# Optimization experiments

Hardware: AMD Instinct MI355X
Metric: run time of the kernel (lower is better)

Reference implementation:

```python
import jax, jax.numpy as jnp
import numpy as np

# static config (Phi-3-like with GQA)
B, S, H, HKV, D, BS = 2, 2048, 32, 8, 128, 64
HID = H * D
NB = B * (S // BS)  # total cache blocks
THETA = 10000.0


def rotate_half(x):
    x1, x2 = jnp.split(x, 2, axis=-1)
    return jnp.concatenate([-x2, x1], axis=-1)


def rope_cos_sin(positions):
    # positions: [T] int -> cos/sin [T, D]
    inv_freq = 1.0 / (THETA ** (jnp.arange(0, D, 2, dtype=jnp.float32) / D))
    freqs = positions.astype(jnp.float32)[:, None] * inv_freq[None, :]
    emb = jnp.concatenate([freqs, freqs], axis=-1)
    return jnp.cos(emb), jnp.sin(emb)


def setup_inputs() -> dict:
    key = jax.random.key(0)
    k1, k2, k3 = jax.random.split(key, 3)
    T = B * S
    hidden_states = jax.random.normal(k1, (T, HID), dtype=jnp.float32)
    w_qkv = jax.random.normal(k2, ((H + 2 * HKV) * D, HID), dtype=jnp.float32) * 0.02
    w_o = jax.random.normal(k3, (HID, H * D), dtype=jnp.float32) * 0.02
    k_cache = jnp.zeros((NB, BS, HKV, D), dtype=jnp.float32)
    v_cache = jnp.zeros((NB, BS, HKV, D), dtype=jnp.float32)
    position_ids = jnp.tile(jnp.arange(S, dtype=jnp.int32), B)  # per-token positions (prefill)
    block_offsets = jnp.arange(NB, dtype=jnp.int32).reshape(B, S // BS)
    return dict(hidden_states=hidden_states, w_qkv=w_qkv, w_o=w_o,
                k_cache=k_cache, v_cache=v_cache, position_ids=position_ids,
                block_offsets=block_offsets, window_size=1024)


def reference(hidden_states, w_qkv, w_o, k_cache, v_cache, position_ids, block_offsets, window_size):
    # fused qkv projection + split
    qkv = hidden_states @ w_qkv.T  # [T, (H+2*HKV)*D]
    q, k, v = jnp.split(qkv, [H * D, H * D + HKV * D], axis=-1)
    q = q.reshape(-1, H, D)
    k = k.reshape(-1, HKV, D)
    v = v.reshape(-1, HKV, D)

    # rotary embedding on flattened tokens
    cos, sin = rope_cos_sin(position_ids)  # [T, D]
    cos, sin = cos[:, None, :], sin[:, None, :]
    q = q * cos + rotate_half(q) * sin
    k = k * cos + rotate_half(k) * sin

    # fill paged KV cache: token t of seq b -> block block_offsets[b, t//BS], slot t%BS
    flat_blocks = block_offsets.reshape(-1)  # [NB]
    k_blk = k.reshape(NB, BS, HKV, D)
    v_blk = v.reshape(NB, BS, HKV, D)
    k_cache = k_cache.at[flat_blocks].set(k_blk)
    v_cache = v_cache.at[flat_blocks].set(v_blk)

    # paged attention: gather per-sequence K/V through the block table
    k_seq = k_cache[block_offsets].reshape(B, S, HKV, D)
    v_seq = v_cache[block_offsets].reshape(B, S, HKV, D)

    G = H // HKV  # query heads per kv head (GQA)
    qh = q.reshape(B, S, HKV, G, D)
    scale = 1.0 / jnp.sqrt(jnp.float32(D))
    scores = jnp.einsum('bshgd,bthd->bhgst', qh, k_seq) * scale  # [B,HKV,G,S,S]

    # causal + sliding-window mask: j <= i and i - j < window_size
    i = jnp.arange(S)[:, None]
    j = jnp.arange(S)[None, :]
    mask = (j <= i) & ((i - j) < window_size)  # [S,S]
    scores = jnp.where(mask[None, None, None], scores, jnp.finfo(scores.dtype).min)
    probs = jax.nn.softmax(scores, axis=-1)

    out = jnp.einsum('bhgst,bthd->bshgd', probs, v_seq)  # [B,S,HKV,G,D]
    out = out.reshape(B * S, H * D)
    return out @ w_o.T  # [T, HID]
```

## Files before the change

### kernel.cpp

```cpp
#include <hip/hip_runtime.h>
#include <hip/hip_bf16.h>
#include <stdint.h>

typedef unsigned short u16;
typedef __attribute__((ext_vector_type(8))) short short8;
typedef __attribute__((ext_vector_type(8))) unsigned short u16x8;
typedef __attribute__((ext_vector_type(4))) float f32x4;

#define B_    2
#define S_    2048
#define H_    32
#define HKV_  8
#define D_    128
#define HID_  4096
#define QKVW_ 6144

__device__ __forceinline__ u16 f2bf(float f){
  uint32_t b = __builtin_bit_cast(uint32_t, f);
  b += 0x7FFFu + ((b >> 16) & 1u);
  return (u16)(b >> 16);
}
__device__ __forceinline__ float bf2f(u16 h){
  uint32_t b = ((uint32_t)h) << 16;
  return __builtin_bit_cast(float, b);
}
__device__ __forceinline__ u16 bfc(float f){
  __hip_bfloat16 h = __float2bfloat16(f);
  return __builtin_bit_cast(u16, h);
}

__device__ __forceinline__ void gload16(const u16* g, u16* l){
  __builtin_amdgcn_global_load_lds((const __attribute__((address_space(1))) void*)g,
                                   (__attribute__((address_space(3))) void*)l, 16, 0, 0);
}

__global__ void cvt_kernel(const float* __restrict__ src, u16* __restrict__ dst, int n4){
  int i = blockIdx.x * blockDim.x + threadIdx.x;
  int stride = gridDim.x * blockDim.x;
  for (; i < n4; i += stride){
    float4 v = reinterpret_cast<const float4*>(src)[i];
    union { u16 u[4]; unsigned long long ll; } o;
    o.u[0] = f2bf(v.x); o.u[1] = f2bf(v.y); o.u[2] = f2bf(v.z); o.u[3] = f2bf(v.w);
    reinterpret_cast<unsigned long long*>(dst)[i] = o.ll;
  }
}

__global__ void rope_table_kernel(float2* __restrict__ tab){
  int idx = blockIdx.x * blockDim.x + threadIdx.x;
  if (idx >= S_ * 64) return;
  int pos = idx >> 6, p = idx & 63;
  float inv = powf(10000.0f, -(float)p / 64.0f);
  float ang = (float)pos * inv;
  tab[idx] = make_float2(cosf(ang), sinf(ang));
}

__global__ void rope_k_kernel(u16* __restrict__ qkv, const int* __restrict__ pos_ids,
                              const float2* __restrict__ tab){
  int t = blockIdx.x;
  int pos = pos_ids[t];
  const float2* tb = tab + pos * 64;
  u16* row = qkv + (size_t)t * QKVW_ + HID_;
  for (int it = threadIdx.x; it < HKV_ * 64; it += 256){
    int hh = it >> 6, p = it & 63;
    int base = hh * D_;
    float x1 = bf2f(row[base + p]);
    float x2 = bf2f(row[base + 64 + p]);
    float2 cs = tb[p];
    row[base + p]      = f2bf(x1 * cs.x - x2 * cs.y);
    row[base + 64 + p] = f2bf(x2 * cs.x + x1 * cs.y);
  }
}

#define MFMA_(a, b, c) __builtin_amdgcn_mfma_f32_16x16x32_bf16((a), (b), (c), 0, 0, 0)

__global__ __launch_bounds__(256) void gemm128(const u16* __restrict__ A, const u16* __restrict__ B,
                                               u16* __restrict__ C, int M, int N, int K){
  __shared__ u16 As[128*64];
  __shared__ u16 Bs[128*64];
  const int tid  = threadIdx.x;
  const int wave = tid >> 6, lane = tid & 63;
  const int hi = lane >> 4, lo = lane & 15;
  const int bn = blockIdx.x, bm = blockIdx.y;
  const int wm = (wave >> 1) * 64, wn = (wave & 1) * 64;
  f32x4 acc[4][4] = {};

  const u16* ap[4]; const u16* bp[4];
  u16* lA[4]; u16* lB[4];
  #pragma unroll
  for (int p = 0; p < 4; p++){
    int e   = p*2048 + wave*512 + lane*8;
    int row = e >> 6;
    int cs  = ((e >> 3) & 7) ^ (row & 7);
    ap[p] = A + (size_t)(bm*128 + row) * K + cs*8;
    bp[p] = B + (size_t)(bn*128 + row) * K + cs*8;
    lA[p] = &As[p*2048 + wave*512];
    lB[p] = &Bs[p*2048 + wave*512];
  }
  const int sw = lo & 7;
  const int nk = K >> 6;
  for (int t = 0; t < nk; t++){
    #pragma unroll
    for (int p = 0; p < 4; p++){
      gload16(ap[p], lA[p]);
      gload16(bp[p], lB[p]);
      ap[p] += 64; bp[p] += 64;
    }
    __syncthreads();
    #pragma unroll
    for (int kk = 0; kk < 2; kk++){
      short8 af[4], bf[4];
      int sz = ((kk*4 + hi) ^ sw) * 8;
      #pragma unroll
      for (int mt = 0; mt < 4; mt++) af[mt] = *(const short8*)&As[(wm + mt*16 + lo)*64 + sz];
      #pragma unroll
      for (int nt = 0; nt < 4; nt++) bf[nt] = *(const short8*)&Bs[(wn + nt*16 + lo)*64 + sz];
      #pragma unroll
      for (int mt = 0; mt < 4; mt++)
        #pragma unroll
        for (int nt = 0; nt < 4; nt++)
          acc[mt][nt] = MFMA_(af[mt], bf[nt], acc[mt][nt]);
    }
    __syncthreads();
  }
  #pragma unroll
  for (int mt = 0; mt < 4; mt++){
    int row = bm*128 + wm + mt*16 + 4*hi;
    #pragma unroll
    for (int nt = 0; nt < 4; nt++){
      int col = bn*128 + wn + nt*16 + lo;
      #pragma unroll
      for (int r = 0; r < 4; r++)
        C[(size_t)(row + r)*N + col] = f2bf(acc[mt][nt][r]);
    }
  }
}

__global__ __launch_bounds__(512, 2) void gemm256(const u16* __restrict__ A, const u16* __restrict__ B,
                                                  float* __restrict__ C, int M, int N, int K, int nbn){
  __shared__ u16 As[2][16384];
  __shared__ u16 Bs[2][16384];
  const int tid = threadIdx.x;
  const int wave = tid >> 6, lane = tid & 63, lo = lane & 15, hi = lane >> 4;
  const int wr = wave >> 2, wc = wave & 3;
  const int sw = lo & 7;

  const int nwg = gridDim.x, bid = blockIdx.x, cpx = nwg >> 3;
  const int wg = (bid & 7) * cpx + (bid >> 3);
  const int bm = wg / nbn, bn = wg - bm * nbn;

  f32x4 acc[8][4] = {};

  const int pr0 = tid >> 3;
  const int sc0 = (tid & 7) ^ (pr0 & 7);
  const u16* aS0 = A + ((size_t)(bm*256 + pr0      ))*K + sc0*8;
  const u16* aS1 = A + ((size_t)(bm*256 + pr0 + 128))*K + sc0*8;
  const u16* aS2 = A + ((size_t)(bm*256 + pr0 + 64 ))*K + sc0*8;
  const u16* aS3 = A + ((size_t)(bm*256 + pr0 + 192))*K + sc0*8;
  const u16* bS0 = B + ((size_t)(bn*256 + pr0      ))*K + sc0*8;
  const u16* bS1 = B + ((size_t)(bn*256 + pr0 + 64 ))*K + sc0*8;
  const u16* bS2 = B + ((size_t)(bn*256 + pr0 + 128))*K + sc0*8;
  const u16* bS3 = B + ((size_t)(bn*256 + pr0 + 192))*K + sc0*8;
  const int dOfs = tid * 8;

  gload16(bS0, &Bs[0][dOfs]);        gload16(bS1, &Bs[0][4096 + dOfs]);
  gload16(bS2, &Bs[0][8192 + dOfs]); gload16(bS3, &Bs[0][12288 + dOfs]);
  gload16(aS0, &As[0][dOfs]);        gload16(aS1, &As[0][4096 + dOfs]);
  gload16(aS2, &As[0][8192 + dOfs]); gload16(aS3, &As[0][12288 + dOfs]);
  asm volatile("s_waitcnt vmcnt(0)" ::: "memory");
  __builtin_amdgcn_s_barrier();

  const int nk = K >> 6;
  for (int t = 0; t < nk; ++t){
    const int cur = t & 1, nxt = cur ^ 1;
    const u16* Ac = &As[cur][0];
    const u16* Bc = &Bs[cur][0];
    u16* An = &As[nxt][0];
    u16* Bn = &Bs[nxt][0];
    const size_t ko = (size_t)(t + 1) * 64;
    const bool more = (t + 1 < nk);
    short8 avr[4], bvr[8];

    #define RD_A(q) \
      _Pragma("unroll") for (int mt = 0; mt < 2; mt++) \
        _Pragma("unroll") for (int kk = 0; kk < 2; kk++){ \
          int ra = wr*128 + (q)*32 + mt*16 + lo; \
          int fo = ((ra & 63) << 6) + ((ra & 64) ? 8192 : 0) + ((ra & 128) ? 4096 : 0) \
                 + ((((kk << 2) + hi) ^ sw) << 3); \
          avr[mt*2 + kk] = *(const short8*)&Ac[fo]; \
        }
    #define DO_MFMA(q) \
      __builtin_amdgcn_s_setprio(1); \
      _Pragma("unroll") for (int mt = 0; mt < 2; mt++) \
        _Pragma("unroll") for (int nt = 0; nt < 4; nt++) \
          _Pragma("unroll") for (int kk = 0; kk < 2; kk++) \
            acc[(q)*2 + mt][nt] = MFMA_(avr[mt*2 + kk], bvr[nt*2 + kk], acc[(q)*2 + mt][nt]); \
      __builtin_amdgcn_s_setprio(0);

    #pragma unroll
    for (int nt = 0; nt < 4; nt++)
      #pragma unroll
      for (int kk = 0; kk < 2; kk++){
        int rb = wc*64 + nt*16 + lo;
        int fo = (rb << 6) + ((((kk << 2) + hi) ^ sw) << 3);
        bvr[nt*2 + kk] = *(const short8*)&Bc[fo];
      }
    RD_A(0)
    if (more){ gload16(bS0 + ko, Bn + dOfs); gload16(bS1 + ko, Bn + 4096 + dOfs); }
    __builtin_amdgcn_s_barrier();
    DO_MFMA(0)
    __builtin_amdgcn_s_barrier();

    RD_A(1)
    if (more){
      gload16(bS2 + ko, Bn + 8192 + dOfs); gload16(bS3 + ko, Bn + 12288 + dOfs);
      asm volatile("s_waitcnt vmcnt(4)" ::: "memory");
    } else {
      asm volatile("s_waitcnt vmcnt(0)" ::: "memory");
    }
    __builtin_amdgcn_sched_barrier(0);
    __builtin_amdgcn_s_barrier();
    DO_MFMA(1)
    __builtin_amdgcn_s_barrier();

    RD_A(2)
    if (more){ gload16(aS0 + ko, An + dOfs); gload16(aS1 + ko, An + 4096 + dOfs); }
    __builtin_amdgcn_s_barrier();
    DO_MFMA(2)
    __builtin_amdgcn_s_barrier();

    RD_A(3)
    if (more){ gload16(aS2 + ko, An + 8192 + dOfs); gload16(aS3 + ko, An + 12288 + dOfs); }
    asm volatile("s_waitcnt vmcnt(2)" ::: "memory");
    __builtin_amdgcn_sched_barrier(0);
    __builtin_amdgcn_s_barrier();
    DO_MFMA(3)
    __builtin_amdgcn_s_barrier();
    #undef RD_A
    #undef DO_MFMA
  }

  #pragma unroll
  for (int mtg = 0; mtg < 8; mtg++){
    int row = bm*256 + wr*128 + mtg*16 + 4*hi;
    #pragma unroll
    for (int nt = 0; nt < 4; nt++){
      int col = bn*256 + wc*64 + nt*16 + lo;
      #pragma unroll
      for (int r = 0; r < 4; r++)
        C[(size_t)(row + r)*N + col] = acc[mtg][nt][r];
    }
  }
}

__global__ __launch_bounds__(256) void attn_kernel(const u16* __restrict__ qkv, u16* __restrict__ out,
                                                   const int* __restrict__ winp,
                                                   const int* __restrict__ pos_ids,
                                                   const float2* __restrict__ tab){
  const int hkv = blockIdx.x, qt = blockIdx.y, z = blockIdx.z;
  const int g = z & 3, b = z >> 2;
  const int h = hkv * 4 + g;
  const int q0 = qt * 64;
  const int tid = threadIdx.x, wave = tid >> 6, lane = tid & 63;
  const int lo = lane & 15, hi = lane >> 4;
  const int win = winp[0];

  __shared__ u16 Ks[2][64*128];
  __shared__ uint32_t VT[2][128*36];
  __shared__ u16 Pl[4][16*72];

  const int qw = q0 + wave*16;
  short8 qf[4];
  {
    const u16* qp = qkv + (size_t)(b*S_ + qw + lo)*QKVW_ + h*D_ + hi*8;
    #pragma unroll
    for (int c = 0; c < 4; c++) qf[c] = *(const short8*)(qp + c*32);
    const float QS = 0.08838834764831845f * 1.4426950408889634f;
    int pos = pos_ids[b*S_ + qw + lo];
    const float2* tb = tab + pos*64 + hi*8;
    #pragma unroll
    for (int i = 0; i < 8; i++){
      float2 csA = tb[i];
      float2 csB = tb[32 + i];
      float x1 = bf2f((u16)qf[0][i]), x2 = bf2f((u16)qf[2][i]);
      qf[0][i] = (short)bfc((x1*csA.x - x2*csA.y) * QS);
      qf[2][i] = (short)bfc((x2*csA.x + x1*csA.y) * QS);
      float y1 = bf2f((u16)qf[1][i]), y2 = bf2f((u16)qf[3][i]);
      qf[1][i] = (short)bfc((y1*csB.x - y2*csB.y) * QS);
      qf[3][i] = (short)bfc((y2*csB.x + y1*csB.y) * QS);
    }
  }

  f32x4 accO[8] = {};
  float m_r = -3.0e38f, l_r = 0.0f;

  int js = q0 - (win - 1); if (js < 0) js = 0; js &= ~63;
  const int nt = (q0 + 64 - js) >> 6;

  const u16* Kg = qkv + (size_t)HID_ + hkv*D_;
  const u16* Vg = qkv + (size_t)HID_ + HKV_*D_ + hkv*D_;
  const int jp = tid & 31, d0 = (tid >> 5) * 16;

  const u16* ksrc[4];
  #pragma unroll
  for (int p = 0; p < 4; p++){
    int e = p*256 + tid;
    int row = e >> 4;
    int ss = (e & 15) ^ (row & 7);
    ksrc[p] = Kg + (size_t)(b*S_ + js + row)*QKVW_ + ss*8;
  }
  const u16* vsrc = Vg + (size_t)(b*S_ + js + 2*jp)*QKVW_ + d0;

  u16x8 vr0, vr1, vr2, vr3;
  {
    #pragma unroll
    for (int p = 0; p < 4; p++) gload16(ksrc[p], &Ks[0][p*2048 + wave*512]);
    vr0 = *(const u16x8*)(vsrc);
    vr1 = *(const u16x8*)(vsrc + 8);
    vr2 = *(const u16x8*)(vsrc + QKVW_);
    vr3 = *(const u16x8*)(vsrc + QKVW_ + 8);
    #pragma unroll
    for (int i = 0; i < 8; i++){
      VT[0][(d0+i)*36 + jp]   = (uint32_t)vr0[i] | ((uint32_t)vr2[i] << 16);
      VT[0][(d0+8+i)*36 + jp] = (uint32_t)vr1[i] | ((uint32_t)vr3[i] << 16);
    }
  }
  __syncthreads();

  for (int t = 0; t < nt; t++){
    const int jc = js + t*64;
    const int cur = t & 1, nxt = cur ^ 1;
    const bool more = (t + 1 < nt);
    if (more){
      const size_t adv = (size_t)(t+1) * 64 * QKVW_;
      #pragma unroll
      for (int p = 0; p < 4; p++) gload16(ksrc[p] + adv, &Ks[nxt][p*2048 + wave*512]);
      const u16* vp = vsrc + adv;
      vr0 = *(const u16x8*)(vp);
      vr1 = *(const u16x8*)(vp + 8);
      vr2 = *(const u16x8*)(vp + QKVW_);
      vr3 = *(const u16x8*)(vp + QKVW_ + 8);
    }
    if (jc <= qw + 15 && jc + 63 >= qw - win + 1){
      f32x4 s[4] = {};
      __builtin_amdgcn_s_setprio(1);
      #pragma unroll
      for (int jt = 0; jt < 4; jt++)
        #pragma unroll
        for (int c = 0; c < 4; c++){
          short8 kf = *(const short8*)&Ks[cur][(jt*16+lo)*128 + (((c*4+hi) ^ (lo & 7)) * 8)];
          s[jt] = MFMA_(kf, qf[c], s[jt]);
        }
      __builtin_amdgcn_s_setprio(0);
      const int qa = qw + lo;
      const bool fullv = (jc + 63 <= qw) && (jc >= qw + 16 - win);
      if (!fullv){
        #pragma unroll
        for (int jt = 0; jt < 4; jt++)
          #pragma unroll
          for (int r = 0; r < 4; r++){
            int j = jc + jt*16 + 4*hi + r;
            if (j > qa || qa - j >= win) s[jt][r] = -3.0e38f;
          }
      }
      float mx = s[0][0];
      #pragma unroll
      for (int jt = 0; jt < 4; jt++)
        #pragma unroll
        for (int r = 0; r < 4; r++) mx = fmaxf(mx, s[jt][r]);
      mx = fmaxf(mx, __shfl_xor(mx, 16));
      mx = fmaxf(mx, __shfl_xor(mx, 32));
      if (__any(mx > m_r + 8.0f)){
        float mn = fmaxf(m_r, mx);
        float al = exp2f(m_r - mn);
        m_r = mn; l_r *= al;
        float a0 = __shfl(al, 4*hi+0), a1 = __shfl(al, 4*hi+1);
        float a2 = __shfl(al, 4*hi+2), a3 = __shfl(al, 4*hi+3);
        #pragma unroll
        for (int dt = 0; dt < 8; dt++){
          accO[dt][0] *= a0; accO[dt][1] *= a1;
          accO[dt][2] *= a2; accO[dt][3] *= a3;
        }
      }
      float ps = 0.f;
      #pragma unroll
      for (int jt = 0; jt < 4; jt++){
        float p0, p1, p2, p3;
        if (fullv){
          p0 = exp2f(s[jt][0] - m_r); p1 = exp2f(s[jt][1] - m_r);
          p2 = exp2f(s[jt][2] - m_r); p3 = exp2f(s[jt][3] - m_r);
        } else {
          p0 = s[jt][0] > -1e37f ? exp2f(s[jt][0] - m_r) : 0.f;
          p1 = s[jt][1] > -1e37f ? exp2f(s[jt][1] - m_r) : 0.f;
          p2 = s[jt][2] > -1e37f ? exp2f(s[jt][2] - m_r) : 0.f;
          p3 = s[jt][3] > -1e37f ? exp2f(s[jt][3] - m_r) : 0.f;
        }
        ps += (p0 + p1) + (p2 + p3);
        uint32_t w0 = (uint32_t)bfc(p0) | ((uint32_t)bfc(p1) << 16);
        uint32_t w1 = (uint32_t)bfc(p2) | ((uint32_t)bfc(p3) << 16);
        *(uint64_t*)&Pl[wave][lo*72 + jt*16 + 4*hi] = (uint64_t)w0 | ((uint64_t)w1 << 32);
      }
      ps += __shfl_xor(ps, 16);
      ps += __shfl_xor(ps, 32);
      l_r += ps;
      short8 pa0 = *(const short8*)&Pl[wave][lo*72 + hi*8];
      short8 pa1 = *(const short8*)&Pl[wave][lo*72 + 32 + hi*8];
      const u16* VT16 = (const u16*)&VT[cur][0];
      __builtin_amdgcn_s_setprio(1);
      #pragma unroll
      for (int dt = 0; dt < 8; dt++){
        short8 vf0 = *(const short8*)&VT16[(dt*16+lo)*72 + hi*8];
        short8 vf1 = *(const short8*)&VT16[(dt*16+lo)*72 + 32 + hi*8];
        accO[dt] = MFMA_(pa0, vf0, accO[dt]);
        accO[dt] = MFMA_(pa1, vf1, accO[dt]);
      }
      __builtin_amdgcn_s_setprio(0);
    }
    if (more){
      #pragma unroll
      for (int i = 0; i < 8; i++){
        VT[nxt][(d0+i)*36 + jp]   = (uint32_t)vr0[i] | ((uint32_t)vr2[i] << 16);
        VT[nxt][(d0+8+i)*36 + jp] = (uint32_t)vr1[i] | ((uint32_t)vr3[i] << 16);
      }
      __syncthreads();
    }
  }
  #pragma unroll
  for (int r = 0; r < 4; r++){
    float lr = __shfl(l_r, 4*hi + r);
    float invl = 1.0f / lr;
    int trow = b*S_ + qw + 4*hi + r;
    #pragma unroll
    for (int dt = 0; dt < 8; dt++)
      out[(size_t)trow*HID_ + h*D_ + dt*16 + lo] = f2bf(accO[dt][r] * invl);
  }
}

extern "C" void kernel_launch(void* const* d_in, const int* in_sizes, int n_in,
                              void* d_out, int out_size, void* d_ws, size_t ws_size,
                              hipStream_t stream) {
  const float* hs   = (const float*)d_in[0];
  const float* wqkv = (const float*)d_in[1];
  const float* wo   = (const float*)d_in[2];
  const int* pos  = (const int*)d_in[5];
  const int* winp = (const int*)d_in[7];
  float* out = (float*)d_out;

  u16* hsb = (u16*)d_ws;
  u16* wqb = hsb + (size_t)HID_*HID_;
  u16* wob = wqb + (size_t)QKVW_*HID_;
  u16* qkv = wob + (size_t)HID_*HID_;
  u16* att = qkv + (size_t)(B_*S_)*QKVW_;
  float2* tab = (float2*)(att + (size_t)(B_*S_)*HID_);

  cvt_kernel<<<2048, 256, 0, stream>>>(hs,   hsb, HID_*HID_/4);
  cvt_kernel<<<2048, 256, 0, stream>>>(wqkv, wqb, QKVW_*HID_/4);
  cvt_kernel<<<2048, 256, 0, stream>>>(wo,   wob, HID_*HID_/4);
  rope_table_kernel<<<(S_*64 + 255)/256, 256, 0, stream>>>(tab);
  gemm128<<<dim3(QKVW_/128, (B_*S_)/128), 256, 0, stream>>>(hsb, wqb, qkv, B_*S_, QKVW_, HID_);
  rope_k_kernel<<<B_*S_, 256, 0, stream>>>(qkv, pos, tab);
  attn_kernel<<<dim3(HKV_, S_/64, 8), 256, 0, stream>>>(qkv, att, winp, pos, tab);
  gemm256<<<(B_*S_/256)*(HID_/256), 512, 0, stream>>>(att, wob, out, B_*S_, HID_, HID_, HID_/256);
}
```

Measured before the change: 573.3 us.

## Rewrite attention with 32x32 MFMA tiles and register-resident P fragments

The attention kernel now uses 32x32x16 bf16 MFMAs with each wave owning 32 query rows (128 per block). The softmax probabilities are packed straight into A-operand fragments in registers via v_cvt_pk_bf16_f32 and v_permlane32_swap, so the LDS round-trip for P goes away. The V transpose buffer gets an XOR-swizzled layout, the grid is flattened to 1D with a staggered query-tile order for load balance, and launch bounds request 2 blocks per SM. The aim is fewer LDS operations and more MFMA work per tile, at the cost of higher register pressure and more masked work on diagonal tiles.

```diff
diff --git a/kernel.cpp b/kernel.cpp
--- a/kernel.cpp
+++ b/kernel.cpp
@@ -6,6 +6,7 @@
 typedef __attribute__((ext_vector_type(8))) short short8;
 typedef __attribute__((ext_vector_type(8))) unsigned short u16x8;
 typedef __attribute__((ext_vector_type(4))) float f32x4;
+typedef __attribute__((ext_vector_type(16))) float f32x16;
 
 #define B_    2
 #define S_    2048
@@ -27,6 +28,14 @@
 __device__ __forceinline__ u16 bfc(float f){
   __hip_bfloat16 h = __float2bfloat16(f);
   return __builtin_bit_cast(u16, h);
+}
+__device__ __forceinline__ uint32_t cvtpk(float a, float b){
+  uint32_t r;
+  asm("v_cvt_pk_bf16_f32 %0, %1, %2" : "=v"(r) : "v"(a), "v"(b));
+  return r;
+}
+__device__ __forceinline__ void pl32swap(uint32_t &a, uint32_t &b){
+  asm volatile("v_permlane32_swap_b32 %0, %1" : "+v"(a), "+v"(b));
 }
 
 __device__ __forceinline__ void gload16(const u16* g, u16* l){
@@ -71,7 +80,8 @@
   }
 }
 
-#define MFMA_(a, b, c) __builtin_amdgcn_mfma_f32_16x16x32_bf16((a), (b), (c), 0, 0, 0)
+#define MFMA_(a, b, c)   __builtin_amdgcn_mfma_f32_16x16x32_bf16((a), (b), (c), 0, 0, 0)
+#define MFMA32_(a, b, c) __builtin_amdgcn_mfma_f32_32x32x16_bf16((a), (b), (c), 0, 0, 0)
 
 __global__ __launch_bounds__(256) void gemm128(const u16* __restrict__ A, const u16* __restrict__ B,
                                                u16* __restrict__ C, int M, int N, int K){
@@ -252,49 +262,50 @@
   }
 }
 
-__global__ __launch_bounds__(256) void attn_kernel(const u16* __restrict__ qkv, u16* __restrict__ out,
-                                                   const int* __restrict__ winp,
-                                                   const int* __restrict__ pos_ids,
-                                                   const float2* __restrict__ tab){
-  const int hkv = blockIdx.x, qt = blockIdx.y, z = blockIdx.z;
-  const int g = z & 3, b = z >> 2;
-  const int h = hkv * 4 + g;
-  const int q0 = qt * 64;
+__global__ __launch_bounds__(256, 2) void attn_kernel(const u16* __restrict__ qkv, u16* __restrict__ out,
+                                                      const int* __restrict__ winp,
+                                                      const int* __restrict__ pos_ids,
+                                                      const float2* __restrict__ tab){
+  const int id = blockIdx.x;
+  const int hkv = id & 7;
+  const int qtr = (id >> 3) & 15;
+  const int gb  = id >> 7;
+  const int qt  = (qtr + 3*gb) & 15;
+  const int g = gb & 3, b = gb >> 2;
+  const int h = hkv*4 + g;
+  const int q0 = qt * 128;
   const int tid = threadIdx.x, wave = tid >> 6, lane = tid & 63;
-  const int lo = lane & 15, hi = lane >> 4;
+  const int ql = lane & 31, hl = lane >> 5;
   const int win = winp[0];
 
   __shared__ u16 Ks[2][64*128];
-  __shared__ uint32_t VT[2][128*36];
-  __shared__ u16 Pl[4][16*72];
-
-  const int qw = q0 + wave*16;
-  short8 qf[4];
+  __shared__ u16 VT[2][128*64];
+
+  const int qw = q0 + wave*32;
+  short8 qf[8];
   {
-    const u16* qp = qkv + (size_t)(b*S_ + qw + lo)*QKVW_ + h*D_ + hi*8;
-    #pragma unroll
-    for (int c = 0; c < 4; c++) qf[c] = *(const short8*)(qp + c*32);
+    const u16* qp = qkv + (size_t)(b*S_ + qw + ql)*QKVW_ + h*D_ + hl*8;
+    #pragma unroll
+    for (int c = 0; c < 8; c++) qf[c] = *(const short8*)(qp + c*16);
     const float QS = 0.08838834764831845f * 1.4426950408889634f;
-    int pos = pos_ids[b*S_ + qw + lo];
-    const float2* tb = tab + pos*64 + hi*8;
-    #pragma unroll
-    for (int i = 0; i < 8; i++){
-      float2 csA = tb[i];
-      float2 csB = tb[32 + i];
-      float x1 = bf2f((u16)qf[0][i]), x2 = bf2f((u16)qf[2][i]);
-      qf[0][i] = (short)bfc((x1*csA.x - x2*csA.y) * QS);
-      qf[2][i] = (short)bfc((x2*csA.x + x1*csA.y) * QS);
-      float y1 = bf2f((u16)qf[1][i]), y2 = bf2f((u16)qf[3][i]);
-      qf[1][i] = (short)bfc((y1*csB.x - y2*csB.y) * QS);
-      qf[3][i] = (short)bfc((y2*csB.x + y1*csB.y) * QS);
-    }
-  }
-
-  f32x4 accO[8] = {};
+    int pos = pos_ids[b*S_ + qw + ql];
+    const float2* tb = tab + pos*64 + hl*8;
+    #pragma unroll
+    for (int c = 0; c < 4; c++)
+      #pragma unroll
+      for (int i = 0; i < 8; i++){
+        float2 cs = tb[c*16 + i];
+        float x1 = bf2f((u16)qf[c][i]), x2 = bf2f((u16)qf[c+4][i]);
+        qf[c][i]   = (short)bfc((x1*cs.x - x2*cs.y) * QS);
+        qf[c+4][i] = (short)bfc((x2*cs.x + x1*cs.y) * QS);
+      }
+  }
+
+  f32x16 acc[4] = {};
   float m_r = -3.0e38f, l_r = 0.0f;
 
   int js = q0 - (win - 1); if (js < 0) js = 0; js &= ~63;
-  const int nt = (q0 + 64 - js) >> 6;
+  const int nt = (q0 + 128 - js) >> 6;
 
   const u16* Kg = qkv + (size_t)HID_ + hkv*D_;
   const u16* Vg = qkv + (size_t)HID_ + HKV_*D_ + hkv*D_;
@@ -305,7 +316,7 @@
   for (int p = 0; p < 4; p++){
     int e = p*256 + tid;
     int row = e >> 4;
-    int ss = (e & 15) ^ (row & 7);
+    int ss = (e & 15) ^ (row & 15);
     ksrc[p] = Kg + (size_t)(b*S_ + js + row)*QKVW_ + ss*8;
   }
   const u16* vsrc = Vg + (size_t)(b*S_ + js + 2*jp)*QKVW_ + d0;
@@ -318,10 +329,12 @@
     vr1 = *(const u16x8*)(vsrc + 8);
     vr2 = *(const u16x8*)(vsrc + QKVW_);
     vr3 = *(const u16x8*)(vsrc + QKVW_ + 8);
+    uint32_t* VT32 = (uint32_t*)&VT[0][0];
     #pragma unroll
     for (int i = 0; i < 8; i++){
-      VT[0][(d0+i)*36 + jp]   = (uint32_t)vr0[i] | ((uint32_t)vr2[i] << 16);
-      VT[0][(d0+8+i)*36 + jp] = (uint32_t)vr1[i] | ((uint32_t)vr3[i] << 16);
+      int da = d0 + i, db = d0 + 8 + i;
+      VT32[da*32 + (jp ^ ((da & 7) << 2))] = (uint32_t)vr0[i] | ((uint32_t)vr2[i] << 16);
+      VT32[db*32 + (jp ^ ((db & 7) << 2))] = (uint32_t)vr1[i] | ((uint32_t)vr3[i] << 16);
     }
   }
   __syncthreads();
@@ -340,98 +353,111 @@
       vr2 = *(const u16x8*)(vp + QKVW_);
       vr3 = *(const u16x8*)(vp + QKVW_ + 8);
     }
-    if (jc <= qw + 15 && jc + 63 >= qw - win + 1){
-      f32x4 s[4] = {};
+    if (jc <= qw + 31 && jc + 63 >= qw - win + 1){
+      f32x16 s0 = {}, s1 = {};
+      const int sl = ql & 15;
       __builtin_amdgcn_s_setprio(1);
       #pragma unroll
-      for (int jt = 0; jt < 4; jt++)
-        #pragma unroll
-        for (int c = 0; c < 4; c++){
-          short8 kf = *(const short8*)&Ks[cur][(jt*16+lo)*128 + (((c*4+hi) ^ (lo & 7)) * 8)];
-          s[jt] = MFMA_(kf, qf[c], s[jt]);
-        }
+      for (int c = 0; c < 8; c++){
+        int so = (((c*2 + hl) ^ sl) * 8);
+        short8 k0 = *(const short8*)&Ks[cur][ql*128 + so];
+        short8 k1 = *(const short8*)&Ks[cur][(32 + ql)*128 + so];
+        s0 = MFMA32_(k0, qf[c], s0);
+        s1 = MFMA32_(k1, qf[c], s1);
+      }
       __builtin_amdgcn_s_setprio(0);
-      const int qa = qw + lo;
-      const bool fullv = (jc + 63 <= qw) && (jc >= qw + 16 - win);
+      const int qa = qw + ql;
+      const bool fullv = (jc + 63 <= qw) && (jc >= qw + 32 - win);
       if (!fullv){
         #pragma unroll
-        for (int jt = 0; jt < 4; jt++)
-          #pragma unroll
-          for (int r = 0; r < 4; r++){
-            int j = jc + jt*16 + 4*hi + r;
-            if (j > qa || qa - j >= win) s[jt][r] = -3.0e38f;
-          }
-      }
-      float mx = s[0][0];
-      #pragma unroll
-      for (int jt = 0; jt < 4; jt++)
-        #pragma unroll
-        for (int r = 0; r < 4; r++) mx = fmaxf(mx, s[jt][r]);
-      mx = fmaxf(mx, __shfl_xor(mx, 16));
+        for (int r = 0; r < 16; r++){
+          int j0 = jc + (r&3) + 8*(r>>2) + 4*hl;
+          if (j0 > qa || qa - j0 >= win) s0[r] = -3.0e38f;
+          int j1 = j0 + 32;
+          if (j1 > qa || qa - j1 >= win) s1[r] = -3.0e38f;
+        }
+      }
+      float mx = s0[0];
+      #pragma unroll
+      for (int r = 1; r < 16; r++) mx = fmaxf(mx, s0[r]);
+      #pragma unroll
+      for (int r = 0; r < 16; r++) mx = fmaxf(mx, s1[r]);
       mx = fmaxf(mx, __shfl_xor(mx, 32));
       if (__any(mx > m_r + 8.0f)){
         float mn = fmaxf(m_r, mx);
         float al = exp2f(m_r - mn);
         m_r = mn; l_r *= al;
-        float a0 = __shfl(al, 4*hi+0), a1 = __shfl(al, 4*hi+1);
-        float a2 = __shfl(al, 4*hi+2), a3 = __shfl(al, 4*hi+3);
-        #pragma unroll
-        for (int dt = 0; dt < 8; dt++){
-          accO[dt][0] *= a0; accO[dt][1] *= a1;
-          accO[dt][2] *= a2; accO[dt][3] *= a3;
+        #pragma unroll
+        for (int r = 0; r < 16; r++){
+          float a = __shfl(al, (r&3) + 8*(r>>2) + 4*hl);
+          acc[0][r] *= a; acc[1][r] *= a; acc[2][r] *= a; acc[3][r] *= a;
         }
       }
       float ps = 0.f;
-      #pragma unroll
-      for (int jt = 0; jt < 4; jt++){
-        float p0, p1, p2, p3;
-        if (fullv){
-          p0 = exp2f(s[jt][0] - m_r); p1 = exp2f(s[jt][1] - m_r);
-          p2 = exp2f(s[jt][2] - m_r); p3 = exp2f(s[jt][3] - m_r);
-        } else {
-          p0 = s[jt][0] > -1e37f ? exp2f(s[jt][0] - m_r) : 0.f;
-          p1 = s[jt][1] > -1e37f ? exp2f(s[jt][1] - m_r) : 0.f;
-          p2 = s[jt][2] > -1e37f ? exp2f(s[jt][2] - m_r) : 0.f;
-          p3 = s[jt][3] > -1e37f ? exp2f(s[jt][3] - m_r) : 0.f;
-        }
-        ps += (p0 + p1) + (p2 + p3);
-        uint32_t w0 = (uint32_t)bfc(p0) | ((uint32_t)bfc(p1) << 16);
-        uint32_t w1 = (uint32_t)bfc(p2) | ((uint32_t)bfc(p3) << 16);
-        *(uint64_t*)&Pl[wave][lo*72 + jt*16 + 4*hi] = (uint64_t)w0 | ((uint64_t)w1 << 32);
-      }
-      ps += __shfl_xor(ps, 16);
+      if (fullv){
+        #pragma unroll
+        for (int r = 0; r < 16; r++){
+          s0[r] = exp2f(s0[r] - m_r); s1[r] = exp2f(s1[r] - m_r);
+          ps += s0[r] + s1[r];
+        }
+      } else {
+        #pragma unroll
+        for (int r = 0; r < 16; r++){
+          s0[r] = s0[r] > -1e37f ? exp2f(s0[r] - m_r) : 0.f;
+          s1[r] = s1[r] > -1e37f ? exp2f(s1[r] - m_r) : 0.f;
+          ps += s0[r] + s1[r];
+        }
+      }
       ps += __shfl_xor(ps, 32);
       l_r += ps;
-      short8 pa0 = *(const short8*)&Pl[wave][lo*72 + hi*8];
-      short8 pa1 = *(const short8*)&Pl[wave][lo*72 + 32 + hi*8];
-      const u16* VT16 = (const u16*)&VT[cur][0];
+      short8 pa[4];
+      #define MKFRAG(dst, P, o) { \
+        uint32_t x1 = cvtpk(P[o+0], P[o+1]), x2 = cvtpk(P[o+2], P[o+3]); \
+        uint32_t y1 = cvtpk(P[o+4], P[o+5]), y2 = cvtpk(P[o+6], P[o+7]); \
+        pl32swap(x1, y1); pl32swap(x2, y2); \
+        union { uint32_t w[4]; short8 v; } u_; \
+        u_.w[0] = x1; u_.w[1] = x2; u_.w[2] = y1; u_.w[3] = y2; \
+        dst = u_.v; }
+      MKFRAG(pa[0], s0, 0)
+      MKFRAG(pa[1], s0, 8)
+      MKFRAG(pa[2], s1, 0)
+      MKFRAG(pa[3], s1, 8)
+      #undef MKFRAG
       __builtin_amdgcn_s_setprio(1);
       #pragma unroll
-      for (int dt = 0; dt < 8; dt++){
-        short8 vf0 = *(const short8*)&VT16[(dt*16+lo)*72 + hi*8];
-        short8 vf1 = *(const short8*)&VT16[(dt*16+lo)*72 + 32 + hi*8];
-        accO[dt] = MFMA_(pa0, vf0, accO[dt]);
-        accO[dt] = MFMA_(pa1, vf1, accO[dt]);
+      for (int dt = 0; dt < 4; dt++){
+        const int dr = dt*32 + ql;
+        const u16* vb = &VT[cur][dr*64];
+        const int sb = dr & 7;
+        #pragma unroll
+        for (int ks = 0; ks < 4; ks++){
+          short8 vf = *(const short8*)&vb[(((ks*2 + hl) ^ sb) * 8)];
+          acc[dt] = MFMA32_(pa[ks], vf, acc[dt]);
+        }
       }
       __builtin_amdgcn_s_setprio(0);
     }
     if (more){
+      uint32_t* VT32 = (uint32_t*)&VT[nxt][0];
       #pragma unroll
       for (int i = 0; i < 8; i++){
-        VT[nxt][(d0+i)*36 + jp]   = (uint32_t)vr0[i] | ((uint32_t)vr2[i] << 16);
-        VT[nxt][(d0+8+i)*36 + jp] = (uint32_t)vr1[i] | ((uint32_t)vr3[i] << 16);
+        int da = d0 + i, db = d0 + 8 + i;
+        VT32[da*32 + (jp ^ ((da & 7) << 2))] = (uint32_t)vr0[i] | ((uint32_t)vr2[i] << 16);
+        VT32[db*32 + (jp ^ ((db & 7) << 2))] = (uint32_t)vr1[i] | ((uint32_t)vr3[i] << 16);
       }
       __syncthreads();
     }
   }
   #pragma unroll
-  for (int r = 0; r < 4; r++){
-    float lr = __shfl(l_r, 4*hi + r);
+  for (int r = 0; r < 16; r++){
+    int qrow = (r&3) + 8*(r>>2) + 4*hl;
+    float lr = __shfl(l_r, qrow);
     float invl = 1.0f / lr;
-    int trow = b*S_ + qw + 4*hi + r;
-    #pragma unroll
-    for (int dt = 0; dt < 8; dt++)
-      out[(size_t)trow*HID_ + h*D_ + dt*16 + lo] = f2bf(accO[dt][r] * invl);
+    size_t ro = (size_t)(b*S_ + qw + qrow)*HID_ + h*D_ + ql;
+    out[ro     ] = f2bf(acc[0][r] * invl);
+    out[ro + 32] = f2bf(acc[1][r] * invl);
+    out[ro + 64] = f2bf(acc[2][r] * invl);
+    out[ro + 96] = f2bf(acc[3][r] * invl);
   }
 }
 
@@ -458,6 +484,6 @@
   rope_table_kernel<<<(S_*64 + 255)/256, 256, 0, stream>>>(tab);
   gemm128<<<dim3(QKVW_/128, (B_*S_)/128), 256, 0, stream>>>(hsb, wqb, qkv, B_*S_, QKVW_, HID_);
   rope_k_kernel<<<B_*S_, 256, 0, stream>>>(qkv, pos, tab);
-  attn_kernel<<<dim3(HKV_, S_/64, 8), 256, 0, stream>>>(qkv, att, winp, pos, tab);
+  attn_kernel<<<1024, 256, 0, stream>>>(qkv, att, winp, pos, tab);
   gemm256<<<(B_*S_/256)*(HID_/256), 512, 0, stream>>>(att, wob, out, B_*S_, HID_, HID_, HID_/256);
 }
```

After: 524.7 us. -8.5%, faster.
